# Performance work log

Hardware: AMD Instinct MI355X
Metric: run time of the kernel (lower is better)

## Reference

```python
import jax, jax.numpy as jnp
import numpy as np

N_SRC = 100000
N_TGT = 100000
N_EDGES = 1600000
D = 128
HID = 128
OUT = 64
NUM_LAYERS = 2
P_DROP = 0.1
NEG_SLOPE = 0.01


def setup_inputs() -> dict:
    key = jax.random.key(0)
    ks = jax.random.split(key, 16)
    s = 1.0 / np.sqrt(D)
    inp = {
        "x_source": jax.random.normal(ks[0], (N_SRC, D), jnp.float32),
        "x_target": jax.random.normal(ks[1], (N_TGT, D), jnp.float32),
        "Wl_tgt": jax.random.normal(ks[2], (NUM_LAYERS, D, HID), jnp.float32) * s,
        "bl_tgt": jax.random.normal(ks[3], (NUM_LAYERS, HID), jnp.float32) * s,
        "Wr_tgt": jax.random.normal(ks[4], (NUM_LAYERS, D, HID), jnp.float32) * s,
        "Wl_src": jax.random.normal(ks[5], (NUM_LAYERS, D, HID), jnp.float32) * s,
        "bl_src": jax.random.normal(ks[6], (NUM_LAYERS, HID), jnp.float32) * s,
        "Wr_src": jax.random.normal(ks[7], (NUM_LAYERS, D, HID), jnp.float32) * s,
        "W_out": jax.random.normal(ks[8], (HID, OUT), jnp.float32) * (1.0 / np.sqrt(HID)),
        "b_out": jax.random.normal(ks[9], (OUT,), jnp.float32) * 0.01,
        "edge_src": jax.random.randint(ks[10], (N_EDGES,), 0, N_SRC, jnp.int32),
        "edge_dst": jax.random.randint(ks[11], (N_EDGES,), 0, N_TGT, jnp.int32),
        "rev_src": jax.random.randint(ks[12], (N_EDGES,), 0, N_TGT, jnp.int32),
        "rev_dst": jax.random.randint(ks[13], (N_EDGES,), 0, N_SRC, jnp.int32),
    }
    return inp


def _sage(x_src, x_dst, src_idx, dst_idx, n_dst, Wl, bl, Wr):
    # mean-aggregate neighbor messages per destination node (PyG SAGEConv default)
    msg = x_src[src_idx]  # [E, D] gather
    agg = jax.ops.segment_sum(msg, dst_idx, num_segments=n_dst)  # [n_dst, D]
    cnt = jax.ops.segment_sum(jnp.ones((src_idx.shape[0],), msg.dtype), dst_idx,
                              num_segments=n_dst)
    mean = agg / jnp.maximum(cnt, 1.0)[:, None]
    return mean @ Wl + bl + x_dst @ Wr


def _dropout(x, key):
    keep = jax.random.bernoulli(key, 1.0 - P_DROP, x.shape)
    return jnp.where(keep, x / (1.0 - P_DROP), jnp.zeros((), x.dtype))


def reference(x_source, x_target, Wl_tgt, bl_tgt, Wr_tgt, Wl_src, bl_src, Wr_src,
              W_out, b_out, edge_src, edge_dst, rev_src, rev_dst):
    dkey = jax.random.key(42)
    xs, xt = x_source, x_target
    for l in range(NUM_LAYERS):
        # ('source','edge','target'): target receives from source
        new_t = _sage(xs, xt, edge_src, edge_dst, N_TGT, Wl_tgt[l], bl_tgt[l], Wr_tgt[l])
        # ('target','rev_edge','source'): source receives from target
        new_s = _sage(xt, xs, rev_src, rev_dst, N_SRC, Wl_src[l], bl_src[l], Wr_src[l])
        new_t = jax.nn.leaky_relu(new_t, NEG_SLOPE)
        new_s = jax.nn.leaky_relu(new_s, NEG_SLOPE)
        new_t = _dropout(new_t, jax.random.fold_in(dkey, 2 * l))
        new_s = _dropout(new_s, jax.random.fold_in(dkey, 2 * l + 1))
        xs, xt = new_s, new_t
    return xs @ W_out + b_out
```

## Files before the change

kernel.cpp:

```cpp
#include <hip/hip_runtime.h>
#include <stdint.h>

#define NN 100000
#define NE 1600000
#define DD 128
#define HB 1024
#define G8 12544
#define SUBN 98
#define NSUB 128
#define NND 100352
#define K2 16
#define RCAP 2304

typedef unsigned short u16;
typedef unsigned long long u64;
typedef short short8 __attribute__((ext_vector_type(8)));
typedef float floatx4 __attribute__((ext_vector_type(4)));
typedef int intx4 __attribute__((ext_vector_type(4)));

__device__ static inline u16 f2bf(float f){
  unsigned u = __float_as_uint(f);
  unsigned r = u + 0x7FFFu + ((u >> 16) & 1u);
  return (u16)(r >> 16);
}

__host__ __device__ static inline unsigned rotl32(unsigned x, int r){
  return (x << r) | (x >> (32 - r));
}

__host__ __device__ static inline void tf2x32(unsigned k0, unsigned k1,
                                              unsigned c0, unsigned c1,
                                              unsigned &o0, unsigned &o1)
{
  const unsigned ks2 = k0 ^ k1 ^ 0x1BD11BDAu;
  unsigned x0 = c0 + k0, x1 = c1 + k1;
#define TFR(r) { x0 += x1; x1 = rotl32(x1, (r)); x1 ^= x0; }
  TFR(13) TFR(15) TFR(26) TFR(6)   x0 += k1;  x1 += ks2 + 1u;
  TFR(17) TFR(29) TFR(16) TFR(24)  x0 += ks2; x1 += k0 + 2u;
  TFR(13) TFR(15) TFR(26) TFR(6)   x0 += k0;  x1 += k1 + 3u;
  TFR(17) TFR(29) TFR(16) TFR(24)  x0 += k1;  x1 += ks2 + 4u;
  TFR(13) TFR(15) TFR(26) TFR(6)   x0 += ks2; x1 += k0 + 5u;
#undef TFR
  o0 = x0; o1 = x1;
}

__device__ static inline int drop_keep(unsigned k0, unsigned k1, unsigned j)
{
  unsigned o0, o1;
  tf2x32(k0, k1, 0u, j, o0, o1);
  const unsigned bits = o0 ^ o1;
  const float u = __uint_as_float((bits >> 9) | 0x3F800000u) - 1.0f;
  return u < 0.9f;
}

__global__ __launch_bounds__(256) void k_hist(const int* __restrict__ e_dst,
                                              const int* __restrict__ r_dst,
                                              int* __restrict__ hist){
  __shared__ int h[16];
  const int t = threadIdx.x;
  if (t < 16) h[t] = 0;
  __syncthreads();
  const int QT = 2 * (NE / 4);
  for (int i = blockIdx.x * 256 + t; i < QT; i += HB * 256){
    int dir = (i >= NE / 4);
    int qi = dir ? i - NE / 4 : i;
    const int* dp = dir ? r_dst : e_dst;
    intx4 d = __builtin_nontemporal_load((const intx4*)dp + qi);
    int bb = dir << 3;
    atomicAdd(&h[bb + d.x / G8], 1);
    atomicAdd(&h[bb + d.y / G8], 1);
    atomicAdd(&h[bb + d.z / G8], 1);
    atomicAdd(&h[bb + d.w / G8], 1);
  }
  __syncthreads();
  if (t < 16) hist[t * HB + blockIdx.x] = h[t];
}

__global__ __launch_bounds__(256) void k_scanA(int* __restrict__ hist){
  __shared__ int sh[16 * HB];
  __shared__ int tot[256];
  const int t = threadIdx.x;
  const int N = 16 * HB;
  for (int k = t; k < N; k += 256) sh[k] = hist[k];
  __syncthreads();
  int s = 0;
  #pragma unroll 4
  for (int k = 0; k < 64; ++k)
    s += sh[(t >> 4) * HB + (t & 15) + (k << 4)];
  tot[t] = s;
  __syncthreads();
  int v = s;
  for (int off = 1; off < 256; off <<= 1){
    int u = (t >= off) ? tot[t - off] : 0;
    __syncthreads();
    tot[t] += u;
    __syncthreads();
  }
  int run = tot[t] - v;
  for (int k = 0; k < 64; ++k){
    int idx = (t >> 4) * HB + (t & 15) + (k << 4);
    int xv = sh[idx];
    sh[idx] = run;
    run += xv;
  }
  __syncthreads();
  for (int k = t; k < N; k += 256) hist[k] = sh[k];
  if (t == 255) hist[N] = tot[255];
}

__global__ __launch_bounds__(256) void k_scatter1(const int* __restrict__ e_src,
                                                  const int* __restrict__ e_dst,
                                                  const int* __restrict__ r_src,
                                                  const int* __restrict__ r_dst,
                                                  const int* __restrict__ base,
                                                  unsigned* __restrict__ stage){
  __shared__ int cur[16];
  const int t = threadIdx.x;
  if (t < 16) cur[t] = base[t * HB + blockIdx.x];
  __syncthreads();
  const int QT = 2 * (NE / 4);
  for (int i = blockIdx.x * 256 + t; i < QT; i += HB * 256){
    int dir = (i >= NE / 4);
    int qi = dir ? i - NE / 4 : i;
    const int* dp = dir ? r_dst : e_dst;
    const int* sp = dir ? r_src : e_src;
    intx4 d = __builtin_nontemporal_load((const intx4*)dp + qi);
    intx4 sv = __builtin_nontemporal_load((const intx4*)sp + qi);
    int bb = dir << 3;
    int g, p;
    g = d.x / G8; p = atomicAdd(&cur[bb + g], 1);
    stage[p] = (unsigned)sv.x | ((unsigned)(d.x - g * G8) << 17);
    g = d.y / G8; p = atomicAdd(&cur[bb + g], 1);
    stage[p] = (unsigned)sv.y | ((unsigned)(d.y - g * G8) << 17);
    g = d.z / G8; p = atomicAdd(&cur[bb + g], 1);
    stage[p] = (unsigned)sv.z | ((unsigned)(d.z - g * G8) << 17);
    g = d.w / G8; p = atomicAdd(&cur[bb + g], 1);
    stage[p] = (unsigned)sv.w | ((unsigned)(d.w - g * G8) << 17);
  }
}

__global__ __launch_bounds__(256) void k_hist2(const unsigned* __restrict__ stage,
                                               const int* __restrict__ base,
                                               int* __restrict__ hist2){
  __shared__ int h2[NSUB];
  const int b16 = blockIdx.x / K2, k = blockIdx.x % K2;
  const int t = threadIdx.x;
  if (t < NSUB) h2[t] = 0;
  __syncthreads();
  const int beg = base[b16 * HB];
  const int end = base[(b16 + 1) * HB];
  for (int i = beg + k * 256 + t; i < end; i += K2 * 256){
    unsigned p = stage[i];
    atomicAdd(&h2[(int)(p >> 17) / SUBN], 1);
  }
  __syncthreads();
  if (t < NSUB) hist2[(b16 * NSUB + t) * K2 + k] = h2[t];
}

__global__ __launch_bounds__(256) void k_scanB(int* __restrict__ hist2){
  __shared__ int sh[16 * NSUB * K2];
  __shared__ int tot[256];
  const int t = threadIdx.x;
  const int N = 16 * NSUB * K2;
  for (int k = t; k < N; k += 256) sh[k] = hist2[k];
  __syncthreads();
  int s = 0;
  for (int j = 0; j < 128; ++j) s += sh[t * 128 + j];
  tot[t] = s;
  __syncthreads();
  int v = s;
  for (int off = 1; off < 256; off <<= 1){
    int u = (t >= off) ? tot[t - off] : 0;
    __syncthreads();
    tot[t] += u;
    __syncthreads();
  }
  int run = tot[t] - v;
  for (int j = 0; j < 128; ++j){
    int xv = sh[t * 128 + j];
    sh[t * 128 + j] = run;
    run += xv;
  }
  __syncthreads();
  for (int k = t; k < N; k += 256) hist2[k] = sh[k];
}

__global__ __launch_bounds__(256) void k_scatter2(const unsigned* __restrict__ stage,
                                                  const int* __restrict__ base,
                                                  const int* __restrict__ h2s,
                                                  unsigned* __restrict__ stage2){
  __shared__ int cur[NSUB];
  const int b16 = blockIdx.x / K2, k = blockIdx.x % K2;
  const int t = threadIdx.x;
  if (t < NSUB) cur[t] = h2s[(b16 * NSUB + t) * K2 + k];
  __syncthreads();
  const int beg = base[b16 * HB];
  const int end = base[(b16 + 1) * HB];
  for (int i = beg + k * 256 + t; i < end; i += K2 * 256){
    unsigned p = stage[i];
    int pos = atomicAdd(&cur[(int)(p >> 17) / SUBN], 1);
    stage2[pos] = p;
  }
}

__global__ __launch_bounds__(256) void k_fill4(const unsigned* __restrict__ stage2,
                                               const int* __restrict__ h2s,
                                               int* __restrict__ ptr,
                                               int* __restrict__ csr){
  __shared__ unsigned rec[RCAP];
  __shared__ unsigned srt[RCAP];
  __shared__ int ldeg[SUBN], lptr[SUBN], lcur[SUBN];
  const int sb = blockIdx.x;
  const int b16 = sb >> 7, sub = sb & 127;
  const int dir = b16 >> 3, g = b16 & 7;
  const int t = threadIdx.x;
  const int beg = h2s[sb * K2];
  const int end = (sb == 2047) ? 2 * NE : h2s[(sb + 1) * K2];
  int n = end - beg;
  if (n > RCAP) n = RCAP;
  for (int i = t; i < n; i += 256) rec[i] = stage2[beg + i];
  if (t < SUBN) ldeg[t] = 0;
  __syncthreads();
  const int nl0 = sub * SUBN;
  for (int i = t; i < n; i += 256)
    atomicAdd(&ldeg[(int)(rec[i] >> 17) - nl0], 1);
  __syncthreads();
  if (t == 0){
    int run = 0;
    for (int s = 0; s < SUBN; ++s){ lptr[s] = run; lcur[s] = run; run += ldeg[s]; }
  }
  __syncthreads();
  for (int i = t; i < n; i += 256){
    int rl = (int)(rec[i] >> 17) - nl0;
    int pos = atomicAdd(&lcur[rl], 1);
    srt[pos] = rec[i] & 0x1FFFFu;
  }
  __syncthreads();
  const int node0 = g * G8 + nl0;
  if (t < SUBN) ptr[dir * NND + node0 + t] = beg + lptr[t];
  if (sb == 2047 && t == 0) ptr[2 * NND] = 2 * NE;
  for (int i = t; i < n; i += 256) csr[beg + i] = (int)srt[i];
}

__global__ __launch_bounds__(256) void k_cvt2(const float* __restrict__ ina,
                                              const float* __restrict__ inb,
                                              u16* __restrict__ oa,
                                              u16* __restrict__ ob, int n8){
  int i = blockIdx.x * 256 + threadIdx.x;
  const float* in = ina; u16* out = oa;
  if (i >= n8){ i -= n8; in = inb; out = ob; }
  floatx4 a = __builtin_nontemporal_load((const floatx4*)in + (size_t)i * 2);
  floatx4 b = __builtin_nontemporal_load((const floatx4*)in + (size_t)i * 2 + 1);
  u16 v[8] = { f2bf(a[0]), f2bf(a[1]), f2bf(a[2]), f2bf(a[3]),
               f2bf(b[0]), f2bf(b[1]), f2bf(b[2]), f2bf(b[3]) };
  *(uint4*)(out + (size_t)i * 8) = *(const uint4*)v;
}

__global__ __launch_bounds__(256) void k_prep(const float* __restrict__ Wl_tgt,
    const float* __restrict__ Wr_tgt, const float* __restrict__ Wl_src,
    const float* __restrict__ Wr_src, const float* __restrict__ Wo,
    u16* __restrict__ Wsw0, u16* __restrict__ Wsw1, u16* __restrict__ Wsw2,
    u16* __restrict__ Wswo){
  int b = blockIdx.x;
  if (b < 48){
    const float *Wl, *Wr; u16* dst;
    if (b < 16){ Wl = Wl_tgt; Wr = Wr_tgt; dst = Wsw0; }
    else if (b < 32){ Wl = Wl_src; Wr = Wr_src; dst = Wsw1; b -= 16; }
    else { Wl = Wl_src + 16384; Wr = Wr_src + 16384; dst = Wsw2; b -= 32; }
    int idx = b * 256 + threadIdx.x;
    int lane = idx & 63, tile = idx >> 6;
    int kt = tile >> 3, nt = tile & 7;
    int n = nt * 16 + (lane & 15);
    int kb = kt * 32 + (lane >> 4) * 8;
    u16 v[8];
    #pragma unroll
    for (int j = 0; j < 8; ++j){
      int k = kb + j;
      float w = (k < 128) ? Wl[(size_t)k * 128 + n] : Wr[(size_t)(k - 128) * 128 + n];
      v[j] = f2bf(w);
    }
    *(uint4*)(dst + (size_t)idx * 8) = *(const uint4*)v;
  } else {
    int idx = (b - 48) * 256 + threadIdx.x;
    int lane = idx & 63, tile = idx >> 6;
    int kt = tile >> 2, nt = tile & 3;
    int n = nt * 16 + (lane & 15);
    int kb = kt * 32 + (lane >> 4) * 8;
    u16 v[8];
    #pragma unroll
    for (int j = 0; j < 8; ++j)
      v[j] = f2bf(Wo[(size_t)(kb + j) * 64 + n]);
    *(uint4*)(Wswo + (size_t)idx * 8) = *(const uint4*)v;
  }
}

__device__ static inline void agg_body(const u16* __restrict__ x,
                                       const int* __restrict__ pd,
                                       const int* __restrict__ csr,
                                       u16* __restrict__ out,
                                       u64* __restrict__ msk,
                                       unsigned key0, unsigned key1, int blk){
  const int row = blk * 4 + (threadIdx.x >> 6);
  const int lane = threadIdx.x & 63;
  const int sub = lane >> 4, l4 = lane & 15;
  const int beg = pd[row], end = pd[row + 1];
  const int cnt = end - beg;
  float a[8] = {0.f,0.f,0.f,0.f,0.f,0.f,0.f,0.f};
  int e = 0;
  for (; e + 7 < cnt; e += 8){
    int s0 = csr[beg + e + sub];
    int s1 = csr[beg + e + 4 + sub];
    uint4 v0 = *(const uint4*)(x + (size_t)s0 * DD + l4 * 8);
    uint4 v1 = *(const uint4*)(x + (size_t)s1 * DD + l4 * 8);
    a[0] += __uint_as_float(v0.x << 16); a[1] += __uint_as_float(v0.x & 0xFFFF0000u);
    a[2] += __uint_as_float(v0.y << 16); a[3] += __uint_as_float(v0.y & 0xFFFF0000u);
    a[4] += __uint_as_float(v0.z << 16); a[5] += __uint_as_float(v0.z & 0xFFFF0000u);
    a[6] += __uint_as_float(v0.w << 16); a[7] += __uint_as_float(v0.w & 0xFFFF0000u);
    a[0] += __uint_as_float(v1.x << 16); a[1] += __uint_as_float(v1.x & 0xFFFF0000u);
    a[2] += __uint_as_float(v1.y << 16); a[3] += __uint_as_float(v1.y & 0xFFFF0000u);
    a[4] += __uint_as_float(v1.z << 16); a[5] += __uint_as_float(v1.z & 0xFFFF0000u);
    a[6] += __uint_as_float(v1.w << 16); a[7] += __uint_as_float(v1.w & 0xFFFF0000u);
  }
  for (; e + 3 < cnt; e += 4){
    int s0 = csr[beg + e + sub];
    uint4 v0 = *(const uint4*)(x + (size_t)s0 * DD + l4 * 8);
    a[0] += __uint_as_float(v0.x << 16); a[1] += __uint_as_float(v0.x & 0xFFFF0000u);
    a[2] += __uint_as_float(v0.y << 16); a[3] += __uint_as_float(v0.y & 0xFFFF0000u);
    a[4] += __uint_as_float(v0.z << 16); a[5] += __uint_as_float(v0.z & 0xFFFF0000u);
    a[6] += __uint_as_float(v0.w << 16); a[7] += __uint_as_float(v0.w & 0xFFFF0000u);
  }
  if (e + sub < cnt){
    int s0 = csr[beg + e + sub];
    uint4 v0 = *(const uint4*)(x + (size_t)s0 * DD + l4 * 8);
    a[0] += __uint_as_float(v0.x << 16); a[1] += __uint_as_float(v0.x & 0xFFFF0000u);
    a[2] += __uint_as_float(v0.y << 16); a[3] += __uint_as_float(v0.y & 0xFFFF0000u);
    a[4] += __uint_as_float(v0.z << 16); a[5] += __uint_as_float(v0.z & 0xFFFF0000u);
    a[6] += __uint_as_float(v0.w << 16); a[7] += __uint_as_float(v0.w & 0xFFFF0000u);
  }
  u64 mA = __ballot(drop_keep(key0, key1, (unsigned)row * 128u + (unsigned)lane));
  u64 mB = __ballot(drop_keep(key0, key1, (unsigned)row * 128u + 64u + (unsigned)lane));
  #pragma unroll
  for (int i = 0; i < 8; ++i){
    a[i] += __shfl_xor(a[i], 16);
    a[i] += __shfl_xor(a[i], 32);
  }
  const float inv = (cnt > 0) ? (1.0f / (float)cnt) : 1.0f;
  if (lane < 2) msk[(size_t)row * 2 + lane] = lane ? mB : mA;
  if (sub == 0){
    unsigned pk[4];
    #pragma unroll
    for (int i = 0; i < 4; ++i)
      pk[i] = (unsigned)f2bf(a[2*i] * inv) | ((unsigned)f2bf(a[2*i+1] * inv) << 16);
    *(uint4*)(out + (size_t)row * DD + l4 * 8) = make_uint4(pk[0], pk[1], pk[2], pk[3]);
  }
}

__global__ __launch_bounds__(256) void k_aggD(const u16* __restrict__ x0,
    const u16* __restrict__ x1, const int* __restrict__ ptr,
    const int* __restrict__ csr, u16* __restrict__ o0, u16* __restrict__ o1,
    u64* __restrict__ m0, u64* __restrict__ m1,
    unsigned k00, unsigned k01, unsigned k10, unsigned k11){
  int b = blockIdx.x;
  if (b < NN / 4) agg_body(x0, ptr, csr, o0, m0, k00, k01, b);
  else            agg_body(x1, ptr + NND, csr, o1, m1, k10, k11, b - NN / 4);
}

__global__ __launch_bounds__(256) void k_agg1(const u16* __restrict__ x,
    const int* __restrict__ ptr, const int* __restrict__ csr,
    u16* __restrict__ out, u64* __restrict__ msk,
    unsigned key0, unsigned key1){
  agg_body(x, ptr + NND, csr, out, msk, key0, key1, blockIdx.x);
}

__device__ static inline void fused_body(const u16* __restrict__ Am,
    const u16* __restrict__ X, const u16* __restrict__ Wsw,
    const float* __restrict__ bias, u16* __restrict__ outH,
    const u64* __restrict__ msk, int blk)
{
  const int wave = threadIdx.x >> 6, lane = threadIdx.x & 63;
  const int quad = lane >> 4, col0 = lane & 15;
  const int row0 = blk * 64 + wave * 16;
  int m = row0 + col0;
  if (m >= NN) m = NN - 1;

  floatx4 acc[8];
  #pragma unroll
  for (int i = 0; i < 8; ++i) acc[i] = (floatx4)0.f;

  #pragma unroll
  for (int kt = 0; kt < 8; ++kt){
    const int k = kt * 32 + quad * 8;
    const u16* ap = (k < 128) ? (Am + (size_t)m * 128 + k)
                              : (X  + (size_t)m * 128 + (k - 128));
    short8 a = __builtin_nontemporal_load((const short8*)ap);
    #pragma unroll
    for (int nt = 0; nt < 8; ++nt){
      short8 b = *(const short8*)(Wsw + (size_t)(((kt * 8 + nt) * 64 + lane) * 8));
      acc[nt] = __builtin_amdgcn_mfma_f32_16x16x32_bf16(a, b, acc[nt], 0, 0, 0);
    }
  }

  u64 w0[4], w1[4];
  #pragma unroll
  for (int rg = 0; rg < 4; ++rg){
    int r = row0 + quad * 4 + rg;
    size_t rr = (size_t)((r < NN) ? r : (NN - 1)) * 2;
    w0[rg] = msk[rr];
    w1[rg] = msk[rr + 1];
  }

  #pragma unroll
  for (int nt = 0; nt < 8; ++nt){
    const int col = nt * 16 + col0;
    const float bj = bias[col];
    const int sh = col & 63;
    #pragma unroll
    for (int rg = 0; rg < 4; ++rg){
      const int r = row0 + quad * 4 + rg;
      if (r < NN){
        float h = acc[nt][rg] + bj;
        h = (h >= 0.f) ? h : 0.01f * h;
        u64 w = (nt < 4) ? w0[rg] : w1[rg];
        h = ((w >> sh) & 1ull) ? h * (1.0f / 0.9f) : 0.0f;
        outH[(size_t)r * 128 + col] = f2bf(h);
      }
    }
  }
}

#define GB ((NN + 63) / 64)

__global__ __launch_bounds__(256) void k_fusedD(
    const u16* __restrict__ A0, const u16* __restrict__ X0,
    const u16* __restrict__ W0, const float* __restrict__ b0,
    u16* __restrict__ o0, const u64* __restrict__ m0,
    const u16* __restrict__ A1, const u16* __restrict__ X1,
    const u16* __restrict__ W1, const float* __restrict__ b1,
    u16* __restrict__ o1, const u64* __restrict__ m1)
{
  int b = blockIdx.x;
  if (b < GB) fused_body(A0, X0, W0, b0, o0, m0, b);
  else        fused_body(A1, X1, W1, b1, o1, m1, b - GB);
}

__global__ __launch_bounds__(256) void k_fused(const u16* __restrict__ Am,
    const u16* __restrict__ X, const u16* __restrict__ Wsw,
    const float* __restrict__ bias, u16* __restrict__ outH,
    const u64* __restrict__ msk)
{
  fused_body(Am, X, Wsw, bias, outH, msk, blockIdx.x);
}

__global__ __launch_bounds__(256) void k_out(const u16* __restrict__ H,
    const u16* __restrict__ Wsw, const float* __restrict__ bias,
    float* __restrict__ out)
{
  const int wave = threadIdx.x >> 6, lane = threadIdx.x & 63;
  const int quad = lane >> 4, col0 = lane & 15;
  const int row0 = blockIdx.x * 64 + wave * 16;
  int m = row0 + col0;
  if (m >= NN) m = NN - 1;

  floatx4 acc[4];
  #pragma unroll
  for (int i = 0; i < 4; ++i) acc[i] = (floatx4)0.f;

  #pragma unroll
  for (int kt = 0; kt < 4; ++kt){
    short8 a = __builtin_nontemporal_load(
        (const short8*)(H + (size_t)m * 128 + kt * 32 + quad * 8));
    #pragma unroll
    for (int nt = 0; nt < 4; ++nt){
      short8 b = *(const short8*)(Wsw + (size_t)(((kt * 4 + nt) * 64 + lane) * 8));
      acc[nt] = __builtin_amdgcn_mfma_f32_16x16x32_bf16(a, b, acc[nt], 0, 0, 0);
    }
  }

  #pragma unroll
  for (int nt = 0; nt < 4; ++nt){
    const int col = nt * 16 + col0;
    const float bj = bias[col];
    #pragma unroll
    for (int rg = 0; rg < 4; ++rg){
      const int r = row0 + quad * 4 + rg;
      if (r < NN)
        out[(size_t)r * 64 + col] = acc[nt][rg] + bj;
    }
  }
}

extern "C" void kernel_launch(void* const* d_in, const int* in_sizes, int n_in,
                              void* d_out, int out_size, void* d_ws, size_t ws_size,
                              hipStream_t stream)
{
  const float* x_src  = (const float*)d_in[0];
  const float* x_tgt  = (const float*)d_in[1];
  const float* Wl_tgt = (const float*)d_in[2];
  const float* bl_tgt = (const float*)d_in[3];
  const float* Wr_tgt = (const float*)d_in[4];
  const float* Wl_src = (const float*)d_in[5];
  const float* bl_src = (const float*)d_in[6];
  const float* Wr_src = (const float*)d_in[7];
  const float* W_o    = (const float*)d_in[8];
  const float* b_o    = (const float*)d_in[9];
  const int*   e_src  = (const int*)d_in[10];
  const int*   e_dst  = (const int*)d_in[11];
  const int*   r_src  = (const int*)d_in[12];
  const int*   r_dst  = (const int*)d_in[13];
  float* out = (float*)d_out;
  (void)in_sizes; (void)n_in; (void)out_size; (void)ws_size;

  char* ws = (char*)d_ws;
  size_t off = 0;
  auto alloc = [&](size_t bytes) -> char* {
    char* p = ws + off; off += (bytes + 255) & ~(size_t)255; return p;
  };
  unsigned* stage1 = (unsigned*)alloc((size_t)2 * NE * 4);
  unsigned* stage2 = (unsigned*)alloc((size_t)2 * NE * 4);
  u16* A_t  = (u16*)stage1;
  u16* A_s  = (u16*)alloc((size_t)NN * DD * 2);
  u16* Xs   = (u16*)alloc((size_t)NN * DD * 2);
  u16* Xt   = (u16*)alloc((size_t)NN * DD * 2);
  u16* B    = (u16*)alloc((size_t)NN * DD * 2);
  u16* C    = (u16*)alloc((size_t)NN * DD * 2);
  u16* Wsw0 = (u16*)alloc(256 * 128 * 2);
  u16* Wsw1 = (u16*)alloc(256 * 128 * 2);
  u16* Wsw2 = (u16*)alloc(256 * 128 * 2);
  u16* Wswo = (u16*)alloc(128 * 64 * 2);
  int* csr  = (int*)alloc((size_t)2 * NE * 4);
  int* ptr  = (int*)alloc((size_t)(2 * NND + 1) * 4);
  int* hist  = (int*)alloc((size_t)(16 * HB + 1) * 4);
  int* hist2 = (int*)alloc((size_t)(16 * NSUB * K2) * 4);
  u64* M0t  = (u64*)alloc((size_t)NN * 2 * 8);
  u64* M0s  = (u64*)alloc((size_t)NN * 2 * 8);
  u64* M1s  = (u64*)alloc((size_t)NN * 2 * 8);

  unsigned kt0a, kt0b, ks0a, ks0b, ks1a, ks1b;
  tf2x32(0u, 42u, 0u, 0u, kt0a, kt0b);
  tf2x32(0u, 42u, 0u, 1u, ks0a, ks0b);
  tf2x32(0u, 42u, 0u, 3u, ks1a, ks1b);

  const int CB = NN * DD / 8 / 256;

  k_cvt2<<<2 * CB, 256, 0, stream>>>(x_src, x_tgt, Xs, Xt, NN * DD / 8);
  k_prep<<<52, 256, 0, stream>>>(Wl_tgt, Wr_tgt, Wl_src, Wr_src, W_o,
                                 Wsw0, Wsw1, Wsw2, Wswo);

  k_hist<<<HB, 256, 0, stream>>>(e_dst, r_dst, hist);
  k_scanA<<<1, 256, 0, stream>>>(hist);
  k_scatter1<<<HB, 256, 0, stream>>>(e_src, e_dst, r_src, r_dst, hist, stage1);
  k_hist2<<<16 * K2, 256, 0, stream>>>(stage1, hist, hist2);
  k_scanB<<<1, 256, 0, stream>>>(hist2);
  k_scatter2<<<16 * K2, 256, 0, stream>>>(stage1, hist, hist2, stage2);
  k_fill4<<<2048, 256, 0, stream>>>(stage2, hist2, ptr, csr);

  const int AB = NN / 4;
  k_aggD<<<2 * AB, 256, 0, stream>>>(Xs, Xt, ptr, csr, A_t, A_s,
                                     M0t, M0s, kt0a, kt0b, ks0a, ks0b);
  k_fusedD<<<2 * GB, 256, 0, stream>>>(A_t, Xt, Wsw0, bl_tgt, B, M0t,
                                       A_s, Xs, Wsw1, bl_src, C, M0s);
  k_agg1<<<AB, 256, 0, stream>>>(B, ptr, csr, A_t, M1s, ks1a, ks1b);
  k_fused<<<GB, 256, 0, stream>>>(A_t, C, Wsw2, bl_src + 128, B, M1s);
  k_out<<<GB, 256, 0, stream>>>(B, Wswo, b_o, out);
}
```

Baseline: 568.9 us.

## Merge prep kernels and overlap layer-0 dropout mask generation with CSR scatter

The fp32-to-bf16 conversion, weight swizzle and destination histogram kernels are merged into one launch. Layer-0 dropout mask generation moves out of the aggregation kernel into extra blocks interleaved with the two latency-bound scatter kernels, so the Threefry hashing runs alongside low-occupancy CSR building. The aggregation accumulation now uses float2 vector adds, which may allow packed FP32 adds. This cuts launches and hashing work from the gather-heavy kernel, at the cost of more complex block indexing and heavier scatter kernels.

```diff
diff --git a/kernel.cpp b/kernel.cpp
--- a/kernel.cpp
+++ b/kernel.cpp
@@ -11,11 +11,13 @@
 #define NND 100352
 #define K2 16
 #define RCAP 2304
+#define MSKB 1563
 
 typedef unsigned short u16;
 typedef unsigned long long u64;
 typedef short short8 __attribute__((ext_vector_type(8)));
 typedef float floatx4 __attribute__((ext_vector_type(4)));
+typedef float floatx2 __attribute__((ext_vector_type(2)));
 typedef int intx4 __attribute__((ext_vector_type(4)));
 
 __device__ static inline u16 f2bf(float f){
@@ -53,27 +55,94 @@
   return u < 0.9f;
 }
 
-__global__ __launch_bounds__(256) void k_hist(const int* __restrict__ e_dst,
-                                              const int* __restrict__ r_dst,
-                                              int* __restrict__ hist){
-  __shared__ int h[16];
+__device__ static inline void mask_body(u64* __restrict__ mp,
+                                        unsigned kk0, unsigned kk1, int mb){
+  const int wave = threadIdx.x >> 6, lane = threadIdx.x & 63;
+  const int base = mb * 64 + wave * 16;
+  for (int i2 = 0; i2 < 16; ++i2){
+    int r = base + i2;
+    if (r >= NN) break;
+    u64 mA = __ballot(drop_keep(kk0, kk1, (unsigned)r * 128u + (unsigned)lane));
+    u64 mB = __ballot(drop_keep(kk0, kk1, (unsigned)r * 128u + 64u + (unsigned)lane));
+    if (lane < 2) mp[(size_t)r * 2 + lane] = lane ? mB : mA;
+  }
+}
+
+#define CVB 12500
+__global__ __launch_bounds__(256) void k_pre(
+    const float* __restrict__ ina, const float* __restrict__ inb,
+    u16* __restrict__ oa, u16* __restrict__ ob, int n8,
+    const int* __restrict__ e_dst, const int* __restrict__ r_dst,
+    int* __restrict__ hist,
+    const float* __restrict__ Wl_tgt, const float* __restrict__ Wr_tgt,
+    const float* __restrict__ Wl_src, const float* __restrict__ Wr_src,
+    const float* __restrict__ Wo,
+    u16* __restrict__ Wsw0, u16* __restrict__ Wsw1, u16* __restrict__ Wsw2,
+    u16* __restrict__ Wswo)
+{
+  const int blk = blockIdx.x;
   const int t = threadIdx.x;
-  if (t < 16) h[t] = 0;
-  __syncthreads();
-  const int QT = 2 * (NE / 4);
-  for (int i = blockIdx.x * 256 + t; i < QT; i += HB * 256){
-    int dir = (i >= NE / 4);
-    int qi = dir ? i - NE / 4 : i;
-    const int* dp = dir ? r_dst : e_dst;
-    intx4 d = __builtin_nontemporal_load((const intx4*)dp + qi);
-    int bb = dir << 3;
-    atomicAdd(&h[bb + d.x / G8], 1);
-    atomicAdd(&h[bb + d.y / G8], 1);
-    atomicAdd(&h[bb + d.z / G8], 1);
-    atomicAdd(&h[bb + d.w / G8], 1);
-  }
-  __syncthreads();
-  if (t < 16) hist[t * HB + blockIdx.x] = h[t];
+  if (blk < CVB){
+    int i = blk * 256 + t;
+    const float* in = ina; u16* out = oa;
+    if (i >= n8){ i -= n8; in = inb; out = ob; }
+    floatx4 a = __builtin_nontemporal_load((const floatx4*)in + (size_t)i * 2);
+    floatx4 c = __builtin_nontemporal_load((const floatx4*)in + (size_t)i * 2 + 1);
+    u16 v[8] = { f2bf(a[0]), f2bf(a[1]), f2bf(a[2]), f2bf(a[3]),
+                 f2bf(c[0]), f2bf(c[1]), f2bf(c[2]), f2bf(c[3]) };
+    *(uint4*)(out + (size_t)i * 8) = *(const uint4*)v;
+  } else if (blk < CVB + HB){
+    const int hb = blk - CVB;
+    __shared__ int h[16];
+    if (t < 16) h[t] = 0;
+    __syncthreads();
+    const int QT = 2 * (NE / 4);
+    for (int i = hb * 256 + t; i < QT; i += HB * 256){
+      int dir = (i >= NE / 4);
+      int qi = dir ? i - NE / 4 : i;
+      const int* dp = dir ? r_dst : e_dst;
+      intx4 d = __builtin_nontemporal_load((const intx4*)dp + qi);
+      int bb = dir << 3;
+      atomicAdd(&h[bb + d.x / G8], 1);
+      atomicAdd(&h[bb + d.y / G8], 1);
+      atomicAdd(&h[bb + d.z / G8], 1);
+      atomicAdd(&h[bb + d.w / G8], 1);
+    }
+    __syncthreads();
+    if (t < 16) hist[t * HB + hb] = h[t];
+  } else {
+    int b = blk - CVB - HB;
+    if (b < 48){
+      const float *Wl, *Wr; u16* dst;
+      if (b < 16){ Wl = Wl_tgt; Wr = Wr_tgt; dst = Wsw0; }
+      else if (b < 32){ Wl = Wl_src; Wr = Wr_src; dst = Wsw1; b -= 16; }
+      else { Wl = Wl_src + 16384; Wr = Wr_src + 16384; dst = Wsw2; b -= 32; }
+      int idx = b * 256 + t;
+      int lane = idx & 63, tile = idx >> 6;
+      int kt = tile >> 3, nt = tile & 7;
+      int n = nt * 16 + (lane & 15);
+      int kb = kt * 32 + (lane >> 4) * 8;
+      u16 v[8];
+      #pragma unroll
+      for (int j = 0; j < 8; ++j){
+        int k = kb + j;
+        float w = (k < 128) ? Wl[(size_t)k * 128 + n] : Wr[(size_t)(k - 128) * 128 + n];
+        v[j] = f2bf(w);
+      }
+      *(uint4*)(dst + (size_t)idx * 8) = *(const uint4*)v;
+    } else {
+      int idx = (b - 48) * 256 + t;
+      int lane = idx & 63, tile = idx >> 6;
+      int kt = tile >> 2, nt = tile & 3;
+      int n = nt * 16 + (lane & 15);
+      int kb = kt * 32 + (lane >> 4) * 8;
+      u16 v[8];
+      #pragma unroll
+      for (int j = 0; j < 8; ++j)
+        v[j] = f2bf(Wo[(size_t)(kb + j) * 64 + n]);
+      *(uint4*)(Wswo + (size_t)idx * 8) = *(const uint4*)v;
+    }
+  }
 }
 
 __global__ __launch_bounds__(256) void k_scanA(int* __restrict__ hist){
@@ -113,13 +182,24 @@
                                                   const int* __restrict__ r_src,
                                                   const int* __restrict__ r_dst,
                                                   const int* __restrict__ base,
-                                                  unsigned* __restrict__ stage){
+                                                  unsigned* __restrict__ stage,
+                                                  u64* __restrict__ M0t,
+                                                  unsigned ka, unsigned kb){
+  const int b = blockIdx.x;
+  const int q = b / 5, rm = b % 5;
+  if (rm >= 2){
+    int mb = q * 3 + (rm - 2);
+    if (mb < MSKB) mask_body(M0t, ka, kb, mb);
+    return;
+  }
+  const int sb = q * 2 + rm;
+  if (sb >= HB) return;
   __shared__ int cur[16];
   const int t = threadIdx.x;
-  if (t < 16) cur[t] = base[t * HB + blockIdx.x];
+  if (t < 16) cur[t] = base[t * HB + sb];
   __syncthreads();
   const int QT = 2 * (NE / 4);
-  for (int i = blockIdx.x * 256 + t; i < QT; i += HB * 256){
+  for (int i = sb * 256 + t; i < QT; i += HB * 256){
     int dir = (i >= NE / 4);
     int qi = dir ? i - NE / 4 : i;
     const int* dp = dir ? r_dst : e_dst;
@@ -188,9 +268,20 @@
 __global__ __launch_bounds__(256) void k_scatter2(const unsigned* __restrict__ stage,
                                                   const int* __restrict__ base,
                                                   const int* __restrict__ h2s,
-                                                  unsigned* __restrict__ stage2){
+                                                  unsigned* __restrict__ stage2,
+                                                  u64* __restrict__ M0s,
+                                                  unsigned ka, unsigned kb){
+  const int b = blockIdx.x;
+  const int q = b / 7, rm = b % 7;
+  if (rm >= 1){
+    int mb = q * 6 + (rm - 1);
+    if (mb < MSKB) mask_body(M0s, ka, kb, mb);
+    return;
+  }
+  const int sb = q;
+  if (sb >= 16 * K2) return;
   __shared__ int cur[NSUB];
-  const int b16 = blockIdx.x / K2, k = blockIdx.x % K2;
+  const int b16 = sb / K2, k = sb % K2;
   const int t = threadIdx.x;
   if (t < NSUB) cur[t] = h2s[(b16 * NSUB + t) * K2 + k];
   __syncthreads();
@@ -242,58 +333,7 @@
   for (int i = t; i < n; i += 256) csr[beg + i] = (int)srt[i];
 }
 
-__global__ __launch_bounds__(256) void k_cvt2(const float* __restrict__ ina,
-                                              const float* __restrict__ inb,
-                                              u16* __restrict__ oa,
-                                              u16* __restrict__ ob, int n8){
-  int i = blockIdx.x * 256 + threadIdx.x;
-  const float* in = ina; u16* out = oa;
-  if (i >= n8){ i -= n8; in = inb; out = ob; }
-  floatx4 a = __builtin_nontemporal_load((const floatx4*)in + (size_t)i * 2);
-  floatx4 b = __builtin_nontemporal_load((const floatx4*)in + (size_t)i * 2 + 1);
-  u16 v[8] = { f2bf(a[0]), f2bf(a[1]), f2bf(a[2]), f2bf(a[3]),
-               f2bf(b[0]), f2bf(b[1]), f2bf(b[2]), f2bf(b[3]) };
-  *(uint4*)(out + (size_t)i * 8) = *(const uint4*)v;
-}
-
-__global__ __launch_bounds__(256) void k_prep(const float* __restrict__ Wl_tgt,
-    const float* __restrict__ Wr_tgt, const float* __restrict__ Wl_src,
-    const float* __restrict__ Wr_src, const float* __restrict__ Wo,
-    u16* __restrict__ Wsw0, u16* __restrict__ Wsw1, u16* __restrict__ Wsw2,
-    u16* __restrict__ Wswo){
-  int b = blockIdx.x;
-  if (b < 48){
-    const float *Wl, *Wr; u16* dst;
-    if (b < 16){ Wl = Wl_tgt; Wr = Wr_tgt; dst = Wsw0; }
-    else if (b < 32){ Wl = Wl_src; Wr = Wr_src; dst = Wsw1; b -= 16; }
-    else { Wl = Wl_src + 16384; Wr = Wr_src + 16384; dst = Wsw2; b -= 32; }
-    int idx = b * 256 + threadIdx.x;
-    int lane = idx & 63, tile = idx >> 6;
-    int kt = tile >> 3, nt = tile & 7;
-    int n = nt * 16 + (lane & 15);
-    int kb = kt * 32 + (lane >> 4) * 8;
-    u16 v[8];
-    #pragma unroll
-    for (int j = 0; j < 8; ++j){
-      int k = kb + j;
-      float w = (k < 128) ? Wl[(size_t)k * 128 + n] : Wr[(size_t)(k - 128) * 128 + n];
-      v[j] = f2bf(w);
-    }
-    *(uint4*)(dst + (size_t)idx * 8) = *(const uint4*)v;
-  } else {
-    int idx = (b - 48) * 256 + threadIdx.x;
-    int lane = idx & 63, tile = idx >> 6;
-    int kt = tile >> 2, nt = tile & 3;
-    int n = nt * 16 + (lane & 15);
-    int kb = kt * 32 + (lane >> 4) * 8;
-    u16 v[8];
-    #pragma unroll
-    for (int j = 0; j < 8; ++j)
-      v[j] = f2bf(Wo[(size_t)(kb + j) * 64 + n]);
-    *(uint4*)(Wswo + (size_t)idx * 8) = *(const uint4*)v;
-  }
-}
-
+template<bool WM>
 __device__ static inline void agg_body(const u16* __restrict__ x,
                                        const int* __restrict__ pd,
                                        const int* __restrict__ csr,
@@ -305,47 +345,46 @@
   const int sub = lane >> 4, l4 = lane & 15;
   const int beg = pd[row], end = pd[row + 1];
   const int cnt = end - beg;
-  float a[8] = {0.f,0.f,0.f,0.f,0.f,0.f,0.f,0.f};
+  floatx2 p0 = (floatx2)0.f, p1 = (floatx2)0.f, p2 = (floatx2)0.f, p3 = (floatx2)0.f;
+#define ACC4(v) { \
+    floatx2 t0, t1, t2, t3; \
+    t0[0] = __uint_as_float((v).x << 16); t0[1] = __uint_as_float((v).x & 0xFFFF0000u); \
+    t1[0] = __uint_as_float((v).y << 16); t1[1] = __uint_as_float((v).y & 0xFFFF0000u); \
+    t2[0] = __uint_as_float((v).z << 16); t2[1] = __uint_as_float((v).z & 0xFFFF0000u); \
+    t3[0] = __uint_as_float((v).w << 16); t3[1] = __uint_as_float((v).w & 0xFFFF0000u); \
+    p0 += t0; p1 += t1; p2 += t2; p3 += t3; }
   int e = 0;
   for (; e + 7 < cnt; e += 8){
     int s0 = csr[beg + e + sub];
     int s1 = csr[beg + e + 4 + sub];
     uint4 v0 = *(const uint4*)(x + (size_t)s0 * DD + l4 * 8);
     uint4 v1 = *(const uint4*)(x + (size_t)s1 * DD + l4 * 8);
-    a[0] += __uint_as_float(v0.x << 16); a[1] += __uint_as_float(v0.x & 0xFFFF0000u);
-    a[2] += __uint_as_float(v0.y << 16); a[3] += __uint_as_float(v0.y & 0xFFFF0000u);
-    a[4] += __uint_as_float(v0.z << 16); a[5] += __uint_as_float(v0.z & 0xFFFF0000u);
-    a[6] += __uint_as_float(v0.w << 16); a[7] += __uint_as_float(v0.w & 0xFFFF0000u);
-    a[0] += __uint_as_float(v1.x << 16); a[1] += __uint_as_float(v1.x & 0xFFFF0000u);
-    a[2] += __uint_as_float(v1.y << 16); a[3] += __uint_as_float(v1.y & 0xFFFF0000u);
-    a[4] += __uint_as_float(v1.z << 16); a[5] += __uint_as_float(v1.z & 0xFFFF0000u);
-    a[6] += __uint_as_float(v1.w << 16); a[7] += __uint_as_float(v1.w & 0xFFFF0000u);
+    ACC4(v0);
+    ACC4(v1);
   }
   for (; e + 3 < cnt; e += 4){
     int s0 = csr[beg + e + sub];
     uint4 v0 = *(const uint4*)(x + (size_t)s0 * DD + l4 * 8);
-    a[0] += __uint_as_float(v0.x << 16); a[1] += __uint_as_float(v0.x & 0xFFFF0000u);
-    a[2] += __uint_as_float(v0.y << 16); a[3] += __uint_as_float(v0.y & 0xFFFF0000u);
-    a[4] += __uint_as_float(v0.z << 16); a[5] += __uint_as_float(v0.z & 0xFFFF0000u);
-    a[6] += __uint_as_float(v0.w << 16); a[7] += __uint_as_float(v0.w & 0xFFFF0000u);
+    ACC4(v0);
   }
   if (e + sub < cnt){
     int s0 = csr[beg + e + sub];
     uint4 v0 = *(const uint4*)(x + (size_t)s0 * DD + l4 * 8);
-    a[0] += __uint_as_float(v0.x << 16); a[1] += __uint_as_float(v0.x & 0xFFFF0000u);
-    a[2] += __uint_as_float(v0.y << 16); a[3] += __uint_as_float(v0.y & 0xFFFF0000u);
-    a[4] += __uint_as_float(v0.z << 16); a[5] += __uint_as_float(v0.z & 0xFFFF0000u);
-    a[6] += __uint_as_float(v0.w << 16); a[7] += __uint_as_float(v0.w & 0xFFFF0000u);
-  }
-  u64 mA = __ballot(drop_keep(key0, key1, (unsigned)row * 128u + (unsigned)lane));
-  u64 mB = __ballot(drop_keep(key0, key1, (unsigned)row * 128u + 64u + (unsigned)lane));
+    ACC4(v0);
+  }
+#undef ACC4
+  if (WM){
+    u64 mA = __ballot(drop_keep(key0, key1, (unsigned)row * 128u + (unsigned)lane));
+    u64 mB = __ballot(drop_keep(key0, key1, (unsigned)row * 128u + 64u + (unsigned)lane));
+    if (lane < 2) msk[(size_t)row * 2 + lane] = lane ? mB : mA;
+  }
+  float a[8] = { p0[0], p0[1], p1[0], p1[1], p2[0], p2[1], p3[0], p3[1] };
   #pragma unroll
   for (int i = 0; i < 8; ++i){
     a[i] += __shfl_xor(a[i], 16);
     a[i] += __shfl_xor(a[i], 32);
   }
   const float inv = (cnt > 0) ? (1.0f / (float)cnt) : 1.0f;
-  if (lane < 2) msk[(size_t)row * 2 + lane] = lane ? mB : mA;
   if (sub == 0){
     unsigned pk[4];
     #pragma unroll
@@ -357,19 +396,17 @@
 
 __global__ __launch_bounds__(256) void k_aggD(const u16* __restrict__ x0,
     const u16* __restrict__ x1, const int* __restrict__ ptr,
-    const int* __restrict__ csr, u16* __restrict__ o0, u16* __restrict__ o1,
-    u64* __restrict__ m0, u64* __restrict__ m1,
-    unsigned k00, unsigned k01, unsigned k10, unsigned k11){
+    const int* __restrict__ csr, u16* __restrict__ o0, u16* __restrict__ o1){
   int b = blockIdx.x;
-  if (b < NN / 4) agg_body(x0, ptr, csr, o0, m0, k00, k01, b);
-  else            agg_body(x1, ptr + NND, csr, o1, m1, k10, k11, b - NN / 4);
+  if (b < NN / 4) agg_body<false>(x0, ptr, csr, o0, nullptr, 0u, 0u, b);
+  else            agg_body<false>(x1, ptr + NND, csr, o1, nullptr, 0u, 0u, b - NN / 4);
 }
 
 __global__ __launch_bounds__(256) void k_agg1(const u16* __restrict__ x,
     const int* __restrict__ ptr, const int* __restrict__ csr,
     u16* __restrict__ out, u64* __restrict__ msk,
     unsigned key0, unsigned key1){
-  agg_body(x, ptr + NND, csr, out, msk, key0, key1, blockIdx.x);
+  agg_body<true>(x, ptr + NND, csr, out, msk, key0, key1, blockIdx.x);
 }
 
 __device__ static inline void fused_body(const u16* __restrict__ Am,
@@ -540,23 +577,21 @@
   tf2x32(0u, 42u, 0u, 1u, ks0a, ks0b);
   tf2x32(0u, 42u, 0u, 3u, ks1a, ks1b);
 
-  const int CB = NN * DD / 8 / 256;
-
-  k_cvt2<<<2 * CB, 256, 0, stream>>>(x_src, x_tgt, Xs, Xt, NN * DD / 8);
-  k_prep<<<52, 256, 0, stream>>>(Wl_tgt, Wr_tgt, Wl_src, Wr_src, W_o,
-                                 Wsw0, Wsw1, Wsw2, Wswo);
-
-  k_hist<<<HB, 256, 0, stream>>>(e_dst, r_dst, hist);
+  k_pre<<<CVB + HB + 52, 256, 0, stream>>>(x_src, x_tgt, Xs, Xt, NN * DD / 8,
+                                           e_dst, r_dst, hist,
+                                           Wl_tgt, Wr_tgt, Wl_src, Wr_src, W_o,
+                                           Wsw0, Wsw1, Wsw2, Wswo);
   k_scanA<<<1, 256, 0, stream>>>(hist);
-  k_scatter1<<<HB, 256, 0, stream>>>(e_src, e_dst, r_src, r_dst, hist, stage1);
+  k_scatter1<<<5 * 521, 256, 0, stream>>>(e_src, e_dst, r_src, r_dst, hist,
+                                          stage1, M0t, kt0a, kt0b);
   k_hist2<<<16 * K2, 256, 0, stream>>>(stage1, hist, hist2);
   k_scanB<<<1, 256, 0, stream>>>(hist2);
-  k_scatter2<<<16 * K2, 256, 0, stream>>>(stage1, hist, hist2, stage2);
+  k_scatter2<<<7 * 261, 256, 0, stream>>>(stage1, hist, hist2, stage2,
+                                          M0s, ks0a, ks0b);
   k_fill4<<<2048, 256, 0, stream>>>(stage2, hist2, ptr, csr);
 
   const int AB = NN / 4;
-  k_aggD<<<2 * AB, 256, 0, stream>>>(Xs, Xt, ptr, csr, A_t, A_s,
-                                     M0t, M0s, kt0a, kt0b, ks0a, ks0b);
+  k_aggD<<<2 * AB, 256, 0, stream>>>(Xs, Xt, ptr, csr, A_t, A_s);
   k_fusedD<<<2 * GB, 256, 0, stream>>>(A_t, Xt, Wsw0, bl_tgt, B, M0t,
                                        A_s, Xs, Wsw1, bl_src, C, M0s);
   k_agg1<<<AB, 256, 0, stream>>>(B, ptr, csr, A_t, M1s, ks1a, ks1b);
```

Result: slower. 608.6 us (+7.0%).
